# Kernel tuning notes

Hardware: AMD Instinct MI355X
Metric: run time of the kernel (lower is better)

## Reference

```python
import jax, jax.numpy as jnp
import numpy as np

ALPHA = 0.0005
TAU = 0.2


def setup_inputs() -> dict:
    key = jax.random.key(0)
    k1, k2, k3 = jax.random.split(key, 3)
    x_batch = jax.random.normal(k1, (2048, 4096), dtype=jnp.float32)
    y_batch = jax.random.normal(k2, (2048, 4096), dtype=jnp.float32)
    # conv weight [out_ch, in_ch, kh, kw]; sliced along dim 2 (F = 64)
    conv_w = jax.random.normal(k3, (512, 512, 64, 3), dtype=jnp.float32) * 0.05
    return {"x_batch": x_batch, "y_batch": y_batch, "conv_w": conv_w}


def _diversity_reg(conv_w, tau):
    # slices conv_w[:, :, i, :] flattened -> rows of v: [F, out*in*kw]
    F = conv_w.shape[2]
    v = jnp.transpose(conv_w, (2, 0, 1, 3)).reshape(F, -1)
    norms = jnp.sqrt(jnp.sum(v * v, axis=1))  # [F]
    gram = v @ v.T  # [F, F] -- memory-bound tall-skinny reduction
    sim = gram / (norms[:, None] * norms[None, :])
    eye = jnp.eye(F, dtype=bool)
    # keep iff tau < sim <= 1 and i != j; zeroed entries are detached (constant 0)
    mask = (sim > tau) & (sim <= 1.0) & (~eye)
    return jnp.sum(jnp.where(mask, sim, 0.0))


def reference(x_batch, y_batch, conv_w):
    # loss_function = MSELoss (mean reduction)
    loss_value = jnp.mean((x_batch - y_batch) ** 2)
    reg_value = _diversity_reg(conv_w, TAU)
    return loss_value + ALPHA * reg_value
```

## Files before the change

### kernel.cpp

```cpp
#include <hip/hip_runtime.h>

typedef __attribute__((ext_vector_type(8)))  short   short8;
typedef __attribute__((ext_vector_type(4)))  unsigned uint4v;
typedef __attribute__((ext_vector_type(16))) float   f32x16;
typedef __attribute__((ext_vector_type(4)))  float   f4;

constexpr int GRAM_BLOCKS = 256;
constexpr int MSE_BLOCKS  = 256;
constexpr int BLOCK       = 512;
constexpr int CHUNK_F     = 3072;
constexpr int CPW         = 8;
constexpr int RED_BLOCKS  = 96;
constexpr int MSE_THREADS = MSE_BLOCKS * BLOCK;

constexpr int MSE_OFF  = 0;
constexpr int FLAG_OFF = 256;
constexpr int GF_OFF   = 512;
constexpr int PART_OFF = 4096;

struct F3 { float v[3]; };
struct Chunk { F3 a0[4], a1[4], b0[4], b1[4]; };

__device__ __forceinline__ unsigned pk_bf16(float a, float b) {
  unsigned a2 = __builtin_bit_cast(unsigned, a) + 0x8000u;
  unsigned b2 = __builtin_bit_cast(unsigned, b) + 0x8000u;
  return __builtin_amdgcn_perm(b2, a2, 0x07060302u);
}

__device__ __forceinline__ void load_chunk(const float* __restrict__ W, int c,
                                           int laneoff, Chunk& ch) {
  const float* s = W + (size_t)c * CHUNK_F + laneoff;
#pragma unroll
  for (int bp = 0; bp < 4; ++bp) {
    const float* p = s + bp * 384;
    ch.a0[bp] = *(const F3*)(p);
    ch.a1[bp] = *(const F3*)(p + 96);
    ch.b0[bp] = *(const F3*)(p + 192);
    ch.b1[bp] = *(const F3*)(p + 288);
  }
}

__device__ __forceinline__ void mac_chunk(const Chunk& c, f32x16& a00, f32x16& a01,
                                          f32x16& a11) {
#pragma unroll
  for (int k = 0; k < 3; ++k) {
    unsigned fl[4], fh[4];
#pragma unroll
    for (int bp = 0; bp < 4; ++bp) {
      fl[bp] = pk_bf16(c.a0[bp].v[k], c.b0[bp].v[k]);
      fh[bp] = pk_bf16(c.a1[bp].v[k], c.b1[bp].v[k]);
    }
    uint4v vl = {fl[0], fl[1], fl[2], fl[3]};
    uint4v vh = {fh[0], fh[1], fh[2], fh[3]};
    short8 lo = __builtin_bit_cast(short8, vl);
    short8 hv = __builtin_bit_cast(short8, vh);
    a00 = __builtin_amdgcn_mfma_f32_32x32x16_bf16(lo, lo, a00, 0, 0, 0);
    a01 = __builtin_amdgcn_mfma_f32_32x32x16_bf16(lo, hv, a01, 0, 0, 0);
    a11 = __builtin_amdgcn_mfma_f32_32x32x16_bf16(hv, hv, a11, 0, 0, 0);
  }
}

__global__ __launch_bounds__(BLOCK, 4) void k_a(
    const float* __restrict__ X, const float* __restrict__ Y,
    const float* __restrict__ W, float* __restrict__ ws) {
  __shared__ __align__(16) float red[4][3072];
  const int bid  = blockIdx.x;
  const int tid  = threadIdx.x;
  const int wave = tid >> 6;
  const int lane = tid & 63;

  if (bid >= GRAM_BLOCKS) {
    const unsigned t0 = (unsigned)((bid - GRAM_BLOCKS) * BLOCK + tid);
    const f4* x4 = (const f4*)X;
    const f4* y4 = (const f4*)Y;
    float acc = 0.f;
#pragma unroll 8
    for (int it = 0; it < 16; ++it) {
      unsigned i = t0 + (unsigned)it * (unsigned)MSE_THREADS;
      f4 a = __builtin_nontemporal_load(x4 + i);
      f4 b = __builtin_nontemporal_load(y4 + i);
      float d0 = a[0] - b[0], d1 = a[1] - b[1], d2 = a[2] - b[2], d3 = a[3] - b[3];
      acc += d0 * d0 + d1 * d1 + d2 * d2 + d3 * d3;
    }
#pragma unroll
    for (int o = 32; o; o >>= 1) acc += __shfl_xor(acc, o, 64);
    __shared__ float fsum[8];
    if (lane == 0) fsum[wave] = acc;
    __syncthreads();
    if (tid == 0) {
      float m = 0.f;
#pragma unroll
      for (int wv = 0; wv < 8; ++wv) m += fsum[wv];
      ws[MSE_OFF + bid - GRAM_BLOCKS] = m;
    }
    return;
  }

  const int r    = lane & 31;
  const int hi   = lane >> 5;
  const int laneoff = hi * 1536 + 3 * r;
  const int c0 = (bid * 8 + wave) * CPW;

  f32x16 a00{}, a01{}, a11{};
  Chunk ca, cb;
  load_chunk(W, c0, laneoff, ca);
#pragma unroll
  for (int t = 0; t < CPW; t += 2) {
    load_chunk(W, c0 + t + 1, laneoff, cb);
    mac_chunk(ca, a00, a01, a11);
    if (t + 2 < CPW) load_chunk(W, c0 + t + 2, laneoff, ca);
    mac_chunk(cb, a00, a01, a11);
  }

  if (wave < 4) {
    float* dst = red[wave];
#pragma unroll
    for (int rg = 0; rg < 16; ++rg) {
      dst[       rg * 64 + lane] = a00[rg];
      dst[1024 + rg * 64 + lane] = a01[rg];
      dst[2048 + rg * 64 + lane] = a11[rg];
    }
  }
  __syncthreads();
  if (wave >= 4) {
    float* dst = red[wave - 4];
#pragma unroll
    for (int rg = 0; rg < 16; ++rg) {
      dst[       rg * 64 + lane] += a00[rg];
      dst[1024 + rg * 64 + lane] += a01[rg];
      dst[2048 + rg * 64 + lane] += a11[rg];
    }
  }
  __syncthreads();
  {
    const f4* r0 = (const f4*)&red[0][0];
    const f4* r1 = (const f4*)&red[1][0];
    const f4* r2 = (const f4*)&red[2][0];
    const f4* r3 = (const f4*)&red[3][0];
    f4* p4 = (f4*)(ws + PART_OFF + (size_t)bid * 3072);
#pragma unroll
    for (int q = tid; q < 768; q += BLOCK)
      p4[q] = (r0[q] + r1[q]) + (r2[q] + r3[q]);
  }
}

__global__ __launch_bounds__(256) void k_b(float* __restrict__ ws,
                                           float* __restrict__ out) {
  __shared__ float r2[4][32];
  __shared__ float g[3072];
  __shared__ float n2[64];
  __shared__ float msum_s[4];
  __shared__ float wsum[4];
  const int tid = threadIdx.x;
  const int lane = tid & 63, wv = tid >> 6, el = lane & 31, ph = lane >> 5;
  const int b = blockIdx.x;
  const int w0 = b * 32;
  int* flags = (int*)(ws + FLAG_OFF);

  const float* base = ws + PART_OFF + (size_t)(ph + 2 * wv) * 3072 + w0 + el;
  float acc = 0.f;
#pragma unroll 8
  for (int i = 0; i < 32; ++i) acc += base[(size_t)i * 24576];
  acc += __shfl_xor(acc, 32, 64);
  if (ph == 0) r2[wv][el] = acc;
  __syncthreads();
  if (tid < 32)
    ws[GF_OFF + w0 + tid] = r2[0][tid] + r2[1][tid] + r2[2][tid] + r2[3][tid];
  __syncthreads();
  if (tid == 0) {
    __threadfence();
    __hip_atomic_store(&flags[b], 1, __ATOMIC_RELEASE, __HIP_MEMORY_SCOPE_AGENT);
  }
  if (b != 0) return;

  if (tid < RED_BLOCKS)
    while (__hip_atomic_load(&flags[tid], __ATOMIC_RELAXED,
                             __HIP_MEMORY_SCOPE_AGENT) != 1)
      __builtin_amdgcn_s_sleep(8);
  __syncthreads();
  __threadfence();

  for (int e = tid; e < 3072; e += 256) g[e] = ws[GF_OFF + e];

  float m = ws[MSE_OFF + tid];
#pragma unroll
  for (int o = 32; o; o >>= 1) m += __shfl_xor(m, o, 64);
  if (lane == 0) msum_s[wv] = m;
  __syncthreads();

  if (tid < RED_BLOCKS) flags[tid] = 0;

  for (int e = tid; e < 3072; e += 256) {
    int tl = e >> 10, rg = (e >> 6) & 15, l = e & 63;
    int il = (rg & 3) + 8 * (rg >> 2) + 4 * (l >> 5);
    int jl = l & 31;
    if (tl != 1 && il == jl) n2[il + (tl == 2 ? 32 : 0)] = g[e];
  }
  __syncthreads();

  float local = 0.f;
  for (int e = tid; e < 3072; e += 256) {
    int tl = e >> 10, rg = (e >> 6) & 15, l = e & 63;
    int il = (rg & 3) + 8 * (rg >> 2) + 4 * (l >> 5);
    int jl = l & 31;
    int i, j; float wgt;
    if (tl == 0)      { i = il;      j = jl;      wgt = 1.f; }
    else if (tl == 1) { i = il;      j = jl + 32; wgt = 2.f; }
    else              { i = il + 32; j = jl + 32; wgt = 1.f; }
    if (i != j) {
      float sim = g[e] / sqrtf(n2[i] * n2[j]);
      if (sim > 0.2f && sim <= 1.0f) local += wgt * sim;
    }
  }
#pragma unroll
  for (int o = 32; o; o >>= 1) local += __shfl_xor(local, o, 64);
  if (lane == 0) wsum[wv] = local;
  __syncthreads();
  if (tid == 0) {
    float reg_sum = wsum[0] + wsum[1] + wsum[2] + wsum[3];
    float mse_sum = msum_s[0] + msum_s[1] + msum_s[2] + msum_s[3];
    out[0] = mse_sum * (1.0f / 8388608.0f) + 0.0005f * reg_sum;
  }
}

extern "C" void kernel_launch(void* const* d_in, const int* in_sizes, int n_in,
                              void* d_out, int out_size, void* d_ws, size_t ws_size,
                              hipStream_t stream) {
  const float* X = (const float*)d_in[0];
  const float* Y = (const float*)d_in[1];
  const float* W = (const float*)d_in[2];
  k_a<<<GRAM_BLOCKS + MSE_BLOCKS, BLOCK, 0, stream>>>(X, Y, W, (float*)d_ws);
  k_b<<<RED_BLOCKS, 256, 0, stream>>>((float*)d_ws, (float*)d_out);
}
```

Measured before the change: 58.66 us.

## Fuse gram reduction and finalize into single kernel using flag-based grid sync

Merges the two-kernel pipeline into one launch. Gram blocks publish partials and set flags; the first 96 blocks spin-wait on all gram flags, reduce partial grams, and set a second flag; block 0 waits on MSE and reduction flags and computes the final loss. This removes the second kernel launch and its gap. The cost is spin-wait latency and reliance on all blocks being co-resident to avoid deadlock.

```diff
diff --git a/kernel.cpp b/kernel.cpp
--- a/kernel.cpp
+++ b/kernel.cpp
@@ -7,6 +7,7 @@
 
 constexpr int GRAM_BLOCKS = 256;
 constexpr int MSE_BLOCKS  = 256;
+constexpr int NB          = GRAM_BLOCKS + MSE_BLOCKS;
 constexpr int BLOCK       = 512;
 constexpr int CHUNK_F     = 3072;
 constexpr int CPW         = 8;
@@ -14,9 +15,10 @@
 constexpr int MSE_THREADS = MSE_BLOCKS * BLOCK;
 
 constexpr int MSE_OFF  = 0;
-constexpr int FLAG_OFF = 256;
-constexpr int GF_OFF   = 512;
-constexpr int PART_OFF = 4096;
+constexpr int F1_OFF   = 256;
+constexpr int F2_OFF   = 768;
+constexpr int GF_OFF   = 1024;
+constexpr int PART_OFF = 4608;
 
 struct F3 { float v[3]; };
 struct Chunk { F3 a0[4], a1[4], b0[4], b1[4]; };
@@ -60,14 +62,21 @@
   }
 }
 
-__global__ __launch_bounds__(BLOCK, 4) void k_a(
+__global__ __launch_bounds__(BLOCK, 4) void k_all(
     const float* __restrict__ X, const float* __restrict__ Y,
-    const float* __restrict__ W, float* __restrict__ ws) {
+    const float* __restrict__ W, float* __restrict__ ws,
+    float* __restrict__ out) {
   __shared__ __align__(16) float red[4][3072];
+  __shared__ float r2[8][32];
+  __shared__ float n2[64];
+  __shared__ float fsum[8];
+  __shared__ float wsum[8];
   const int bid  = blockIdx.x;
   const int tid  = threadIdx.x;
   const int wave = tid >> 6;
   const int lane = tid & 63;
+  int* flag1 = (int*)(ws + F1_OFF);
+  int* flag2 = (int*)(ws + F2_OFF);
 
   if (bid >= GRAM_BLOCKS) {
     const unsigned t0 = (unsigned)((bid - GRAM_BLOCKS) * BLOCK + tid);
@@ -84,7 +93,6 @@
     }
 #pragma unroll
     for (int o = 32; o; o >>= 1) acc += __shfl_xor(acc, o, 64);
-    __shared__ float fsum[8];
     if (lane == 0) fsum[wave] = acc;
     __syncthreads();
     if (tid == 0) {
@@ -92,6 +100,8 @@
 #pragma unroll
       for (int wv = 0; wv < 8; ++wv) m += fsum[wv];
       ws[MSE_OFF + bid - GRAM_BLOCKS] = m;
+      __threadfence();
+      __hip_atomic_store(&flag1[bid], 1, __ATOMIC_RELEASE, __HIP_MEMORY_SCOPE_AGENT);
     }
     return;
   }
@@ -135,62 +145,75 @@
   {
     const f4* r0 = (const f4*)&red[0][0];
     const f4* r1 = (const f4*)&red[1][0];
-    const f4* r2 = (const f4*)&red[2][0];
+    const f4* r2v = (const f4*)&red[2][0];
     const f4* r3 = (const f4*)&red[3][0];
     f4* p4 = (f4*)(ws + PART_OFF + (size_t)bid * 3072);
-#pragma unroll
     for (int q = tid; q < 768; q += BLOCK)
-      p4[q] = (r0[q] + r1[q]) + (r2[q] + r3[q]);
-  }
-}
-
-__global__ __launch_bounds__(256) void k_b(float* __restrict__ ws,
-                                           float* __restrict__ out) {
-  __shared__ float r2[4][32];
-  __shared__ float g[3072];
-  __shared__ float n2[64];
-  __shared__ float msum_s[4];
-  __shared__ float wsum[4];
-  const int tid = threadIdx.x;
-  const int lane = tid & 63, wv = tid >> 6, el = lane & 31, ph = lane >> 5;
-  const int b = blockIdx.x;
-  const int w0 = b * 32;
-  int* flags = (int*)(ws + FLAG_OFF);
-
-  const float* base = ws + PART_OFF + (size_t)(ph + 2 * wv) * 3072 + w0 + el;
-  float acc = 0.f;
-#pragma unroll 8
-  for (int i = 0; i < 32; ++i) acc += base[(size_t)i * 24576];
-  acc += __shfl_xor(acc, 32, 64);
-  if (ph == 0) r2[wv][el] = acc;
-  __syncthreads();
-  if (tid < 32)
-    ws[GF_OFF + w0 + tid] = r2[0][tid] + r2[1][tid] + r2[2][tid] + r2[3][tid];
+      p4[q] = (r0[q] + r1[q]) + (r2v[q] + r3[q]);
+  }
   __syncthreads();
   if (tid == 0) {
     __threadfence();
-    __hip_atomic_store(&flags[b], 1, __ATOMIC_RELEASE, __HIP_MEMORY_SCOPE_AGENT);
-  }
-  if (b != 0) return;
-
-  if (tid < RED_BLOCKS)
-    while (__hip_atomic_load(&flags[tid], __ATOMIC_RELAXED,
+    __hip_atomic_store(&flag1[bid], 1, __ATOMIC_RELEASE, __HIP_MEMORY_SCOPE_AGENT);
+  }
+  if (bid >= RED_BLOCKS) return;
+
+  if (tid < GRAM_BLOCKS)
+    while (__hip_atomic_load(&flag1[tid], __ATOMIC_RELAXED,
                              __HIP_MEMORY_SCOPE_AGENT) != 1)
       __builtin_amdgcn_s_sleep(8);
   __syncthreads();
   __threadfence();
 
-  for (int e = tid; e < 3072; e += 256) g[e] = ws[GF_OFF + e];
-
-  float m = ws[MSE_OFF + tid];
+  {
+    const int el = lane & 31, ph = lane >> 5;
+    const int w0 = bid * 32;
+    const float* base = ws + PART_OFF + (size_t)(ph + 2 * wave) * 3072 + w0 + el;
+    float acc = 0.f;
+#pragma unroll
+    for (int i = 0; i < 16; ++i) acc += base[(size_t)i * 49152];
+    acc += __shfl_xor(acc, 32, 64);
+    if (ph == 0) r2[wave][el] = acc;
+    __syncthreads();
+    if (tid < 32) {
+      float s = 0.f;
+#pragma unroll
+      for (int wv = 0; wv < 8; ++wv) s += r2[wv][tid];
+      ws[GF_OFF + w0 + tid] = s;
+    }
+  }
+  __syncthreads();
+  if (tid == 0) {
+    __threadfence();
+    __hip_atomic_store(&flag2[bid], 1, __ATOMIC_RELEASE, __HIP_MEMORY_SCOPE_AGENT);
+  }
+  if (bid != 0) return;
+
+  if (tid < MSE_BLOCKS) {
+    while (__hip_atomic_load(&flag1[GRAM_BLOCKS + tid], __ATOMIC_RELAXED,
+                             __HIP_MEMORY_SCOPE_AGENT) != 1)
+      __builtin_amdgcn_s_sleep(8);
+  } else if (tid < MSE_BLOCKS + RED_BLOCKS) {
+    while (__hip_atomic_load(&flag2[tid - MSE_BLOCKS], __ATOMIC_RELAXED,
+                             __HIP_MEMORY_SCOPE_AGENT) != 1)
+      __builtin_amdgcn_s_sleep(8);
+  }
+  __syncthreads();
+  __threadfence();
+
+  float* g = &red[0][0];
+  for (int e = tid; e < 3072; e += BLOCK) g[e] = ws[GF_OFF + e];
+
+  float m = (tid < MSE_BLOCKS) ? ws[MSE_OFF + tid] : 0.f;
 #pragma unroll
   for (int o = 32; o; o >>= 1) m += __shfl_xor(m, o, 64);
-  if (lane == 0) msum_s[wv] = m;
-  __syncthreads();
-
-  if (tid < RED_BLOCKS) flags[tid] = 0;
-
-  for (int e = tid; e < 3072; e += 256) {
+  if (lane == 0) fsum[wave] = m;
+
+  flag1[tid] = 0;
+  if (tid < RED_BLOCKS) flag2[tid] = 0;
+  __syncthreads();
+
+  for (int e = tid; e < 3072; e += BLOCK) {
     int tl = e >> 10, rg = (e >> 6) & 15, l = e & 63;
     int il = (rg & 3) + 8 * (rg >> 2) + 4 * (l >> 5);
     int jl = l & 31;
@@ -199,7 +222,7 @@
   __syncthreads();
 
   float local = 0.f;
-  for (int e = tid; e < 3072; e += 256) {
+  for (int e = tid; e < 3072; e += BLOCK) {
     int tl = e >> 10, rg = (e >> 6) & 15, l = e & 63;
     int il = (rg & 3) + 8 * (rg >> 2) + 4 * (l >> 5);
     int jl = l & 31;
@@ -214,11 +237,12 @@
   }
 #pragma unroll
   for (int o = 32; o; o >>= 1) local += __shfl_xor(local, o, 64);
-  if (lane == 0) wsum[wv] = local;
+  if (lane == 0) wsum[wave] = local;
   __syncthreads();
   if (tid == 0) {
-    float reg_sum = wsum[0] + wsum[1] + wsum[2] + wsum[3];
-    float mse_sum = msum_s[0] + msum_s[1] + msum_s[2] + msum_s[3];
+    float reg_sum = 0.f, mse_sum = 0.f;
+#pragma unroll
+    for (int wv = 0; wv < 8; ++wv) { reg_sum += wsum[wv]; mse_sum += fsum[wv]; }
     out[0] = mse_sum * (1.0f / 8388608.0f) + 0.0005f * reg_sum;
   }
 }
@@ -229,6 +253,5 @@
   const float* X = (const float*)d_in[0];
   const float* Y = (const float*)d_in[1];
   const float* W = (const float*)d_in[2];
-  k_a<<<GRAM_BLOCKS + MSE_BLOCKS, BLOCK, 0, stream>>>(X, Y, W, (float*)d_ws);
-  k_b<<<RED_BLOCKS, 256, 0, stream>>>((float*)d_ws, (float*)d_out);
-}
+  k_all<<<NB, BLOCK, 0, stream>>>(X, Y, W, (float*)d_ws, (float*)d_out);
+}
```

Result: slower. 94.01 us (+60.3%).

## Co-schedule MSE and Gram work within each block via wave specialization

Applied to the files above, without the earlier changes.

Instead of separate block ranges for the Gram reduction and the MSE, every block now gives 6 waves to Gram chunks (grid-strided across 3072 waves) and 2 waves to MSE streaming. The aim is to mix the two bandwidth streams on every CU and balance the load, rather than relying on block scheduling order. The in-block reduction drops to 3 LDS buffers. The partial count doubles to 512, so the second kernel reads twice as many Gram partials and MSE sums. Gram waves handle an uneven chunk count (16384/3072), which adds tail imbalance.

```diff
diff --git a/kernel.cpp b/kernel.cpp
--- a/kernel.cpp
+++ b/kernel.cpp
@@ -5,17 +5,17 @@
 typedef __attribute__((ext_vector_type(16))) float   f32x16;
 typedef __attribute__((ext_vector_type(4)))  float   f4;
 
-constexpr int GRAM_BLOCKS = 256;
-constexpr int MSE_BLOCKS  = 256;
+constexpr int NB          = 512;
 constexpr int BLOCK       = 512;
+constexpr int GRAM_WPB    = 6;
 constexpr int CHUNK_F     = 3072;
-constexpr int CPW         = 8;
+constexpr int NCHUNK      = 16384;
+constexpr int NGW         = NB * GRAM_WPB;
 constexpr int RED_BLOCKS  = 96;
-constexpr int MSE_THREADS = MSE_BLOCKS * BLOCK;
 
 constexpr int MSE_OFF  = 0;
-constexpr int FLAG_OFF = 256;
-constexpr int GF_OFF   = 512;
+constexpr int FLAG_OFF = 512;
+constexpr int GF_OFF   = 1024;
 constexpr int PART_OFF = 4096;
 
 struct F3 { float v[3]; };
@@ -63,56 +63,54 @@
 __global__ __launch_bounds__(BLOCK, 4) void k_a(
     const float* __restrict__ X, const float* __restrict__ Y,
     const float* __restrict__ W, float* __restrict__ ws) {
-  __shared__ __align__(16) float red[4][3072];
+  __shared__ __align__(16) float red[3][3072];
+  __shared__ float fsum[2];
   const int bid  = blockIdx.x;
   const int tid  = threadIdx.x;
   const int wave = tid >> 6;
   const int lane = tid & 63;
 
-  if (bid >= GRAM_BLOCKS) {
-    const unsigned t0 = (unsigned)((bid - GRAM_BLOCKS) * BLOCK + tid);
+  f32x16 a00{}, a01{}, a11{};
+  float macc = 0.f;
+
+  if (wave >= GRAM_WPB) {
+    const int m = bid * 2 + (wave - GRAM_WPB);
     const f4* x4 = (const f4*)X;
     const f4* y4 = (const f4*)Y;
-    float acc = 0.f;
 #pragma unroll 8
-    for (int it = 0; it < 16; ++it) {
-      unsigned i = t0 + (unsigned)it * (unsigned)MSE_THREADS;
+    for (int it = 0; it < 32; ++it) {
+      unsigned i = (unsigned)it * 65536u + (unsigned)m * 64u + (unsigned)lane;
       f4 a = __builtin_nontemporal_load(x4 + i);
       f4 b = __builtin_nontemporal_load(y4 + i);
       float d0 = a[0] - b[0], d1 = a[1] - b[1], d2 = a[2] - b[2], d3 = a[3] - b[3];
-      acc += d0 * d0 + d1 * d1 + d2 * d2 + d3 * d3;
-    }
-#pragma unroll
-    for (int o = 32; o; o >>= 1) acc += __shfl_xor(acc, o, 64);
-    __shared__ float fsum[8];
-    if (lane == 0) fsum[wave] = acc;
-    __syncthreads();
-    if (tid == 0) {
-      float m = 0.f;
-#pragma unroll
-      for (int wv = 0; wv < 8; ++wv) m += fsum[wv];
-      ws[MSE_OFF + bid - GRAM_BLOCKS] = m;
-    }
-    return;
-  }
-
-  const int r    = lane & 31;
-  const int hi   = lane >> 5;
-  const int laneoff = hi * 1536 + 3 * r;
-  const int c0 = (bid * 8 + wave) * CPW;
-
-  f32x16 a00{}, a01{}, a11{};
-  Chunk ca, cb;
-  load_chunk(W, c0, laneoff, ca);
-#pragma unroll
-  for (int t = 0; t < CPW; t += 2) {
-    load_chunk(W, c0 + t + 1, laneoff, cb);
-    mac_chunk(ca, a00, a01, a11);
-    if (t + 2 < CPW) load_chunk(W, c0 + t + 2, laneoff, ca);
-    mac_chunk(cb, a00, a01, a11);
-  }
-
-  if (wave < 4) {
+      macc += d0 * d0 + d1 * d1 + d2 * d2 + d3 * d3;
+    }
+#pragma unroll
+    for (int o = 32; o; o >>= 1) macc += __shfl_xor(macc, o, 64);
+    if (lane == 0) fsum[wave - GRAM_WPB] = macc;
+  } else {
+    const int r    = lane & 31;
+    const int hi   = lane >> 5;
+    const int laneoff = hi * 1536 + 3 * r;
+    const int g = bid * GRAM_WPB + wave;
+
+    Chunk ca, cb;
+    int c = g;
+    load_chunk(W, c, laneoff, ca);
+    c += NGW;
+    for (;;) {
+      if (c < NCHUNK) load_chunk(W, c, laneoff, cb);
+      mac_chunk(ca, a00, a01, a11);
+      if (c >= NCHUNK) break;
+      c += NGW;
+      if (c < NCHUNK) load_chunk(W, c, laneoff, ca);
+      mac_chunk(cb, a00, a01, a11);
+      if (c >= NCHUNK) break;
+      c += NGW;
+    }
+  }
+
+  if (wave < 3) {
     float* dst = red[wave];
 #pragma unroll
     for (int rg = 0; rg < 16; ++rg) {
@@ -122,8 +120,8 @@
     }
   }
   __syncthreads();
-  if (wave >= 4) {
-    float* dst = red[wave - 4];
+  if (wave >= 3 && wave < 6) {
+    float* dst = red[wave - 3];
 #pragma unroll
     for (int rg = 0; rg < 16; ++rg) {
       dst[       rg * 64 + lane] += a00[rg];
@@ -136,12 +134,12 @@
     const f4* r0 = (const f4*)&red[0][0];
     const f4* r1 = (const f4*)&red[1][0];
     const f4* r2 = (const f4*)&red[2][0];
-    const f4* r3 = (const f4*)&red[3][0];
     f4* p4 = (f4*)(ws + PART_OFF + (size_t)bid * 3072);
 #pragma unroll
     for (int q = tid; q < 768; q += BLOCK)
-      p4[q] = (r0[q] + r1[q]) + (r2[q] + r3[q]);
-  }
+      p4[q] = r0[q] + r1[q] + r2[q];
+  }
+  if (tid == 0) ws[MSE_OFF + bid] = fsum[0] + fsum[1];
 }
 
 __global__ __launch_bounds__(256) void k_b(float* __restrict__ ws,
@@ -160,7 +158,7 @@
   const float* base = ws + PART_OFF + (size_t)(ph + 2 * wv) * 3072 + w0 + el;
   float acc = 0.f;
 #pragma unroll 8
-  for (int i = 0; i < 32; ++i) acc += base[(size_t)i * 24576];
+  for (int i = 0; i < 64; ++i) acc += base[(size_t)i * 24576];
   acc += __shfl_xor(acc, 32, 64);
   if (ph == 0) r2[wv][el] = acc;
   __syncthreads();
@@ -182,7 +180,7 @@
 
   for (int e = tid; e < 3072; e += 256) g[e] = ws[GF_OFF + e];
 
-  float m = ws[MSE_OFF + tid];
+  float m = ws[MSE_OFF + tid] + ws[MSE_OFF + 256 + tid];
 #pragma unroll
   for (int o = 32; o; o >>= 1) m += __shfl_xor(m, o, 64);
   if (lane == 0) msum_s[wv] = m;
@@ -229,6 +227,6 @@
   const float* X = (const float*)d_in[0];
   const float* Y = (const float*)d_in[1];
   const float* W = (const float*)d_in[2];
-  k_a<<<GRAM_BLOCKS + MSE_BLOCKS, BLOCK, 0, stream>>>(X, Y, W, (float*)d_ws);
+  k_a<<<NB, BLOCK, 0, stream>>>(X, Y, W, (float*)d_ws);
   k_b<<<RED_BLOCKS, 256, 0, stream>>>((float*)d_ws, (float*)d_out);
 }
```

Result: slower. 223.3 us (+280.7%).
